# Kernel optimization log

Measured on AMD Instinct MI355X. Metric: run time of the kernel, lower is better.

Reference implementation:

```python
import jax, jax.numpy as jnp
import numpy as np

HIDDEN = 4096
N_HEADS = 32
N_KV_HEADS = 2
HEAD_DIM = 128          # hidden // n_heads
ROT_DIM = HEAD_DIM // 2  # partial rotary (ChatGLM style)
ROPE_THETA = 10000.0
Q_SIZE = N_HEADS * HEAD_DIM
KV_SIZE = N_KV_HEADS * HEAD_DIM
SCALE = HEAD_DIM ** -0.5
T = 2048


def setup_inputs() -> dict:
    key = jax.random.key(0)
    k1, k2, k3, k4 = jax.random.split(key, 4)
    hidden_states = jax.random.normal(k1, (T, HIDDEN), dtype=jnp.float32)
    positions = jnp.arange(T, dtype=jnp.int64) if jax.config.jax_enable_x64 else jnp.arange(T, dtype=jnp.int32)
    w_qkv = jax.random.normal(k2, (Q_SIZE + 2 * KV_SIZE, HIDDEN), dtype=jnp.float32) * 0.02
    b_qkv = jax.random.normal(k3, (Q_SIZE + 2 * KV_SIZE,), dtype=jnp.float32) * 0.02
    w_dense = jax.random.normal(k4, (HIDDEN, Q_SIZE), dtype=jnp.float32) * 0.02
    return {"hidden_states": hidden_states, "positions": positions,
            "w_qkv": w_qkv, "b_qkv": b_qkv, "w_dense": w_dense}


def _apply_rope(x, positions):
    # x: [T, H, HEAD_DIM]; interleaved (is_neox_style=False) partial rotary on first ROT_DIM dims
    half = ROT_DIM // 2
    inv_freq = 1.0 / (ROPE_THETA ** (jnp.arange(0, half, dtype=jnp.float32) * 2.0 / ROT_DIM))
    freqs = positions.astype(jnp.float32)[:, None] * inv_freq[None, :]   # [T, half]
    cos = jnp.cos(freqs)[:, None, :]  # [T, 1, half]
    sin = jnp.sin(freqs)[:, None, :]
    x_rot = x[..., :ROT_DIM]
    x_pass = x[..., ROT_DIM:]
    x1 = x_rot[..., 0::2]
    x2 = x_rot[..., 1::2]
    o1 = x1 * cos - x2 * sin
    o2 = x2 * cos + x1 * sin
    rot = jnp.stack([o1, o2], axis=-1).reshape(x_rot.shape)  # re-interleave
    return jnp.concatenate([rot, x_pass], axis=-1)


def reference(hidden_states, positions, w_qkv, b_qkv, w_dense):
    # QKV projection (bias from add_qkv_bias=True)
    qkv = hidden_states @ w_qkv.T + b_qkv                     # [T, 4608]
    q = qkv[:, :Q_SIZE].reshape(T, N_HEADS, HEAD_DIM)
    k = qkv[:, Q_SIZE:Q_SIZE + KV_SIZE].reshape(T, N_KV_HEADS, HEAD_DIM)
    v = qkv[:, Q_SIZE + KV_SIZE:].reshape(T, N_KV_HEADS, HEAD_DIM)

    q = _apply_rope(q, positions)
    k = _apply_rope(k, positions)

    # GQA: expand 2 kv heads -> 32 q heads (each kv head serves 16 q heads)
    rep = N_HEADS // N_KV_HEADS
    k = jnp.repeat(k, rep, axis=1)                            # [T, 32, 128]
    v = jnp.repeat(v, rep, axis=1)

    # Causal scaled dot-product attention
    scores = jnp.einsum('thd,shd->hts', q, k) * SCALE         # [H, T, T]
    causal = positions[:, None] >= positions[None, :]          # [T, T]
    scores = jnp.where(causal[None, :, :], scores, jnp.finfo(scores.dtype).min)
    probs = jax.nn.softmax(scores, axis=-1)
    attn = jnp.einsum('hts,shd->thd', probs, v).reshape(T, Q_SIZE)

    # Output projection (no bias: add_bias_linear=False)
    return attn @ w_dense.T
```

## Files before the change

kernel.cpp:

```cpp
#include <hip/hip_runtime.h>
#include <cstdint>
#include <math.h>

typedef __bf16 bf16;
typedef __bf16 bf16x8 __attribute__((ext_vector_type(8)));
typedef __bf16 bf16x4 __attribute__((ext_vector_type(4)));
typedef float f32x4 __attribute__((ext_vector_type(4)));

#define T_SEQ 2048
#define HID   4096
#define NQH   32
#define NKVH  2
#define HD    128
#define NQKV  4608
#define ATT_SCALE 0.08838834764831845f

#define VMCNT(n) asm volatile("s_waitcnt vmcnt(" #n ")" ::: "memory")

__device__ __forceinline__ void load_lds16(const void* g, void* l) {
    auto gp = (const __attribute__((address_space(1))) unsigned int*)(uintptr_t)g;
    auto lp = (__attribute__((address_space(3))) unsigned int*)(unsigned int)(uintptr_t)l;
    __builtin_amdgcn_global_load_lds(gp, lp, 16, 0, 0);
}

__device__ __forceinline__ f32x4 mfma16(bf16x8 a, bf16x8 b, f32x4 c) {
    return __builtin_amdgcn_mfma_f32_16x16x32_bf16(a, b, c, 0, 0, 0);
}

__device__ __forceinline__ bf16x8 cvt8(const float* s) {
    float4 a = *(const float4*)(s);
    float4 b = *(const float4*)(s + 4);
    bf16x8 o;
    o[0] = (bf16)a.x; o[1] = (bf16)a.y; o[2] = (bf16)a.z; o[3] = (bf16)a.w;
    o[4] = (bf16)b.x; o[5] = (bf16)b.y; o[6] = (bf16)b.z; o[7] = (bf16)b.w;
    return o;
}

__global__ void cvt2_kernel(const float* __restrict__ s0, bf16* __restrict__ d0, long n0,
                            const float* __restrict__ s1, bf16* __restrict__ d1, long n1) {
    const long nv = (n0 + n1) >> 3;
    for (long v = (long)blockIdx.x * 256 + threadIdx.x; v < nv; v += (long)gridDim.x * 256) {
        long i = v << 3;
        if (i < n0) *(bf16x8*)(d0 + i) = cvt8(s0 + i);
        else        *(bf16x8*)(d1 + (i - n0)) = cvt8(s1 + (i - n0));
    }
}

__global__ void cvt_f32_bf16_kernel(const float* __restrict__ x, bf16* __restrict__ y) {
    size_t i = ((size_t)blockIdx.x * 256 + threadIdx.x) * 8;
    *(bf16x8*)(y + i) = cvt8(x + i);
}

template <int OUT_BF16, int HAS_BIAS>
__global__ __launch_bounds__(256) void gemm_bt(const bf16* __restrict__ A,
                                               const bf16* __restrict__ B,
                                               const float* __restrict__ bias,
                                               void* __restrict__ Cout,
                                               int M, int N, int K) {
    __shared__ __align__(16) char sA[2][16384];
    __shared__ __align__(16) char sB[2][16384];
    const int tid = threadIdx.x;
    const int wid = tid >> 6, l = tid & 63, l4 = l >> 4, l16 = l & 15;
    const int wm = wid >> 1, wn = wid & 1;
    const int bm = blockIdx.x * 128, bn = blockIdx.y * 128;

    f32x4 acc[4][4] = {};

    auto stage = [&](int buf, int k0) {
#pragma unroll
        for (int c4 = 0; c4 < 4; ++c4) {
            int ch = c4 * 256 + tid;
            int row = ch >> 3, cch = ch & 7;
            int scc = cch ^ (row & 7);
            load_lds16(A + (size_t)(bm + row) * K + k0 + scc * 8,
                       sA[buf] + c4 * 4096 + wid * 1024);
        }
#pragma unroll
        for (int c4 = 0; c4 < 4; ++c4) {
            int ch = c4 * 256 + tid;
            int row = ch >> 3, cch = ch & 7;
            int scc = cch ^ (row & 7);
            load_lds16(B + (size_t)(bn + row) * K + k0 + scc * 8,
                       sB[buf] + c4 * 4096 + wid * 1024);
        }
    };

    stage(0, 0);
    const int NT = K >> 6;
    int cur = 0;
    for (int t = 0; t < NT; ++t) {
        __builtin_amdgcn_s_barrier();
        __builtin_amdgcn_sched_barrier(0);
        if (t + 1 < NT) {
            stage(cur ^ 1, (t + 1) * 64);
            VMCNT(8);
        } else {
            VMCNT(0);
        }
        __builtin_amdgcn_s_barrier();
        __builtin_amdgcn_sched_barrier(0);

        const char* pA = sA[cur];
        const char* pB = sB[cur];
#pragma unroll
        for (int ks = 0; ks < 2; ++ks) {
            bf16x8 af[4], bfr[4];
#pragma unroll
            for (int mi = 0; mi < 4; ++mi) {
                int row = wm * 64 + mi * 16 + l16;
                af[mi] = *(const bf16x8*)(pA + row * 128 + ((ks * 64 + l4 * 16) ^ ((row & 7) << 4)));
            }
#pragma unroll
            for (int ni = 0; ni < 4; ++ni) {
                int row = wn * 64 + ni * 16 + l16;
                bfr[ni] = *(const bf16x8*)(pB + row * 128 + ((ks * 64 + l4 * 16) ^ ((row & 7) << 4)));
            }
#pragma unroll
            for (int mi = 0; mi < 4; ++mi)
#pragma unroll
                for (int ni = 0; ni < 4; ++ni)
                    acc[mi][ni] = mfma16(af[mi], bfr[ni], acc[mi][ni]);
        }
        cur ^= 1;
    }

#pragma unroll
    for (int mi = 0; mi < 4; ++mi)
#pragma unroll
        for (int ni = 0; ni < 4; ++ni) {
            const int col = bn + wn * 64 + ni * 16 + l16;
            float bv = HAS_BIAS ? bias[col] : 0.0f;
#pragma unroll
            for (int r = 0; r < 4; ++r) {
                const int row = bm + wm * 64 + mi * 16 + l4 * 4 + r;
                float val = acc[mi][ni][r] + bv;
                if (OUT_BF16)
                    ((bf16*)Cout)[(size_t)row * N + col] = (bf16)val;
                else
                    ((float*)Cout)[(size_t)row * N + col] = val;
            }
        }
}

__global__ void rope_qk_kernel(const bf16* __restrict__ qkv,
                               bf16* __restrict__ qheads, bf16* __restrict__ kheads) {
    const int t = blockIdx.x;
    const int g = blockIdx.y;
    const int sub = threadIdx.x >> 6;
    const int l = threadIdx.x & 63;
    const bf16* src;
    bf16* dst;
    if (g < 8) {
        int hh = g * 4 + sub;
        src = qkv + (size_t)t * NQKV + hh * HD;
        dst = qheads + ((size_t)hh * T_SEQ + t) * HD;
    } else {
        if (sub >= 2) return;
        src = qkv + (size_t)t * NQKV + HID + sub * HD;
        dst = kheads + ((size_t)sub * T_SEQ + t) * HD;
    }
    if (l < 32) {
        const int i = l;
        float x1 = (float)src[2 * i], x2 = (float)src[2 * i + 1];
        float fr = (float)t * exp2f((float)i * (-13.287712379549449f / 32.0f));
        float sn = sinf(fr), cs = cosf(fr);
        dst[2 * i] = (bf16)(x1 * cs - x2 * sn);
        dst[2 * i + 1] = (bf16)(x2 * cs + x1 * sn);
    } else {
        const int j = l - 32;
        dst[64 + 2 * j] = src[64 + 2 * j];
        dst[64 + 2 * j + 1] = src[64 + 2 * j + 1];
    }
}

__global__ void v_trans_kernel(const bf16* __restrict__ qkv, bf16* __restrict__ vt) {
    const int t0 = blockIdx.x * 64;
    const int kvh = blockIdx.y;
    const int tid = threadIdx.x;
#pragma unroll
    for (int it = 0; it < 4; ++it) {
        int ch = it * 256 + tid;
        int d = ch >> 3, tc = ch & 7;
        int t = t0 + tc * 8;
        const bf16* src = qkv + (size_t)t * NQKV + 4352 + kvh * HD + d;
        bf16x8 v;
#pragma unroll
        for (int i = 0; i < 8; ++i) v[i] = src[(size_t)i * NQKV];
        *(bf16x8*)(vt + ((size_t)kvh * HD + d) * T_SEQ + t) = v;
    }
}

__global__ __launch_bounds__(256, 1) void attn_fwd_kernel(const bf16* __restrict__ qh,
                                                          const bf16* __restrict__ kh,
                                                          const bf16* __restrict__ vt,
                                                          bf16* __restrict__ attnb) {
    __shared__ __align__(16) char sK[2][16384];
    __shared__ __align__(16) char sV[16384];
    __shared__ __align__(16) char sP[4][4096];
    const int tid = threadIdx.x;
    const int wid = tid >> 6, l = tid & 63, l4 = l >> 4, l16 = l & 15;
    const int b = blockIdx.x;
    const int qb = 15 - (b >> 5);
    const int h = b & 31, kvh = h >> 4;
    const int qbase = qb * 128 + wid * 32;

    auto stageK = [&](int buf, int kt) {
#pragma unroll
        for (int c4 = 0; c4 < 4; ++c4) {
            int ch = c4 * 256 + tid;
            int row = ch >> 4, cc = ch & 15;
            load_lds16(kh + ((size_t)kvh * T_SEQ + kt * 64 + row) * HD + (cc ^ (row & 7)) * 8,
                       sK[buf] + c4 * 4096 + wid * 1024);
        }
    };
    auto stageV = [&](int kt) {
#pragma unroll
        for (int c4 = 0; c4 < 4; ++c4) {
            int ch = c4 * 256 + tid;
            int row = ch >> 3, cc = ch & 7;
            load_lds16(vt + ((size_t)kvh * HD + row) * T_SEQ + kt * 64 + (cc ^ (row & 7)) * 8,
                       sV + c4 * 4096 + wid * 1024);
        }
    };

    bf16x8 qf[2][4];
#pragma unroll
    for (int rg = 0; rg < 2; ++rg) {
        const bf16* qp = qh + ((size_t)h * T_SEQ + qbase + rg * 16 + l16) * HD + l4 * 8;
#pragma unroll
        for (int f = 0; f < 4; ++f) qf[rg][f] = *(const bf16x8*)(qp + f * 32);
    }
    VMCNT(0);
    stageK(0, 0);

    f32x4 o[2][8] = {};
    float mr[2][4], lr[2][4];
#pragma unroll
    for (int rg = 0; rg < 2; ++rg)
#pragma unroll
        for (int r = 0; r < 4; ++r) { mr[rg][r] = -INFINITY; lr[rg][r] = 0.f; }

    const int nt = 2 * qb + 2;
    int cur = 0;
    for (int kt = 0; kt < nt; ++kt) {
        const bool havenext = (kt + 1 < nt);
        __builtin_amdgcn_s_barrier();
        __builtin_amdgcn_sched_barrier(0);
        stageV(kt);
        if (havenext) stageK(cur ^ 1, kt + 1);
        if (havenext) { VMCNT(16); } else { VMCNT(8); }
        __builtin_amdgcn_s_barrier();
        __builtin_amdgcn_sched_barrier(0);

        const bool active = (kt * 64) <= (qbase + 31);
        if (active) {
            f32x4 s[2][4] = {};
            __builtin_amdgcn_s_setprio(1);
#pragma unroll
            for (int ct = 0; ct < 4; ++ct)
#pragma unroll
                for (int ks = 0; ks < 4; ++ks) {
                    int row = ct * 16 + l16;
                    bf16x8 kf = *(const bf16x8*)(sK[cur] + row * 256 + ((ks * 64 + l4 * 16) ^ ((row & 7) << 4)));
                    s[0][ct] = mfma16(qf[0][ks], kf, s[0][ct]);
                    s[1][ct] = mfma16(qf[1][ks], kf, s[1][ct]);
                }
            __builtin_amdgcn_s_setprio(0);

            const bool diag = (kt * 64 + 63 > qbase);
            float sv[2][4][4];
#pragma unroll
            for (int rg = 0; rg < 2; ++rg)
#pragma unroll
                for (int ct = 0; ct < 4; ++ct)
#pragma unroll
                    for (int r = 0; r < 4; ++r) {
                        float x = s[rg][ct][r] * ATT_SCALE;
                        if (diag && (kt * 64 + ct * 16 + l16) > (qbase + rg * 16 + l4 * 4 + r)) x = -INFINITY;
                        sv[rg][ct][r] = x;
                    }

            float pmx[2][4];
            bool ok = true;
#pragma unroll
            for (int rg = 0; rg < 2; ++rg)
#pragma unroll
                for (int r = 0; r < 4; ++r) {
                    pmx[rg][r] = fmaxf(fmaxf(sv[rg][0][r], sv[rg][1][r]), fmaxf(sv[rg][2][r], sv[rg][3][r]));
                    ok = ok && (pmx[rg][r] <= mr[rg][r] + 8.0f);
                }
            if (!__all(ok)) {
#pragma unroll
                for (int rg = 0; rg < 2; ++rg)
#pragma unroll
                    for (int r = 0; r < 4; ++r) {
                        float mx = pmx[rg][r];
                        mx = fmaxf(mx, __shfl_xor(mx, 1));
                        mx = fmaxf(mx, __shfl_xor(mx, 2));
                        mx = fmaxf(mx, __shfl_xor(mx, 4));
                        mx = fmaxf(mx, __shfl_xor(mx, 8));
                        if (mx > mr[rg][r]) {
                            float al = __expf(mr[rg][r] - mx);
                            mr[rg][r] = mx;
                            lr[rg][r] *= al;
#pragma unroll
                            for (int n2 = 0; n2 < 8; ++n2) o[rg][n2][r] *= al;
                        }
                    }
            }
#pragma unroll
            for (int rg = 0; rg < 2; ++rg)
#pragma unroll
                for (int r = 0; r < 4; ++r) {
                    float ps = 0.f;
                    const int prow = rg * 16 + l4 * 4 + r;
#pragma unroll
                    for (int ct = 0; ct < 4; ++ct) {
                        float p = __expf(sv[rg][ct][r] - mr[rg][r]);
                        ps += p;
                        *(bf16*)(sP[wid] + prow * 128 + (((ct * 16 + l16) * 2) ^ ((prow & 7) << 4))) = (bf16)p;
                    }
                    lr[rg][r] += ps;
                }
        }

        if (havenext) { VMCNT(8); } else { VMCNT(0); }
        __builtin_amdgcn_s_barrier();
        __builtin_amdgcn_sched_barrier(0);

        if (active) {
#pragma unroll
            for (int ks = 0; ks < 2; ++ks) {
                bf16x8 pa0 = *(const bf16x8*)(sP[wid] + l16 * 128 + ((ks * 64 + l4 * 16) ^ ((l16 & 7) << 4)));
                bf16x8 pa1 = *(const bf16x8*)(sP[wid] + (16 + l16) * 128 + ((ks * 64 + l4 * 16) ^ ((l16 & 7) << 4)));
                __builtin_amdgcn_s_setprio(1);
#pragma unroll
                for (int n2 = 0; n2 < 8; ++n2) {
                    int vrow = n2 * 16 + l16;
                    bf16x8 vf = *(const bf16x8*)(sV + vrow * 128 + ((ks * 64 + l4 * 16) ^ ((vrow & 7) << 4)));
                    o[0][n2] = mfma16(pa0, vf, o[0][n2]);
                    o[1][n2] = mfma16(pa1, vf, o[1][n2]);
                }
                __builtin_amdgcn_s_setprio(0);
            }
        }
        cur ^= 1;
    }

    float inv[2][4];
#pragma unroll
    for (int rg = 0; rg < 2; ++rg)
#pragma unroll
        for (int r = 0; r < 4; ++r) {
            float s2 = lr[rg][r];
            s2 += __shfl_xor(s2, 1);
            s2 += __shfl_xor(s2, 2);
            s2 += __shfl_xor(s2, 4);
            s2 += __shfl_xor(s2, 8);
            inv[rg][r] = 1.0f / s2;
        }
#pragma unroll
    for (int rg = 0; rg < 2; ++rg)
#pragma unroll
        for (int n2 = 0; n2 < 8; ++n2)
#pragma unroll
            for (int r = 0; r < 4; ++r) {
                int row = qb * 128 + wid * 32 + rg * 16 + l4 * 4 + r;
                int col = h * HD + n2 * 16 + l16;
                attnb[(size_t)row * HID + col] = (bf16)(o[rg][n2][r] * inv[rg][r]);
            }
}

extern "C" void kernel_launch(void* const* d_in, const int* in_sizes, int n_in,
                              void* d_out, int out_size, void* d_ws, size_t ws_size,
                              hipStream_t stream) {
    const float* hs = (const float*)d_in[0];
    const float* wqkv = (const float*)d_in[2];
    const float* bqkv = (const float*)d_in[3];
    const float* wdense = (const float*)d_in[4];
    float* out = (float*)d_out;

    char* ws = (char*)d_ws;
    bf16* wqkvb   = (bf16*)(ws + 0);
    bf16* hb      = (bf16*)(ws + 37748736);
    bf16* qkvb    = (bf16*)(ws + 54525952);
    bf16* qhp     = (bf16*)(ws + 0);
    bf16* khp     = (bf16*)(ws + 16777216);
    bf16* vtp     = (bf16*)(ws + 17825792);
    bf16* wdenseb = (bf16*)(ws + 18874368);
    bf16* attnb   = (bf16*)(ws + 54525952);
    (void)in_sizes; (void)n_in; (void)out_size; (void)ws_size;

    cvt2_kernel<<<2048, 256, 0, stream>>>(hs, hb, (long)T_SEQ * HID,
                                          wqkv, wqkvb, (long)NQKV * HID);

    dim3 g1(T_SEQ / 128, NQKV / 128);
    gemm_bt<1, 1><<<g1, 256, 0, stream>>>(hb, wqkvb, bqkv, (void*)qkvb, T_SEQ, NQKV, HID);

    cvt_f32_bf16_kernel<<<(HID * HID) / 2048, 256, 0, stream>>>(wdense, wdenseb);

    rope_qk_kernel<<<dim3(T_SEQ, 9), 256, 0, stream>>>(qkvb, qhp, khp);
    v_trans_kernel<<<dim3(T_SEQ / 64, NKVH), 256, 0, stream>>>(qkvb, vtp);

    attn_fwd_kernel<<<512, 256, 0, stream>>>(qhp, khp, vtp, attnb);

    dim3 g2(T_SEQ / 128, HID / 128);
    gemm_bt<0, 0><<<g2, 256, 0, stream>>>(attnb, wdenseb, nullptr, (void*)out, T_SEQ, HID, HID);
}
```

Before: 326.4 us.

## Drop LDS staging in attention, load K/V directly, fuse w_dense conversion

The attention kernel stops staging K and V through double-buffered LDS with barriers. Each wave now loads its K and V fragments straight from global memory into registers and computes a per-wave trip count, so no block-level synchronisation is needed. The separate w_dense f32-to-bf16 conversion kernel is folded into the tail of the attention kernel, saving one launch, and the occupancy hint of one block per CU is dropped. In exchange, K/V tiles that four waves could share are fetched redundantly from global or L2 memory, with no async prefetch to hide the load latency.

```diff
diff --git a/kernel.cpp b/kernel.cpp
--- a/kernel.cpp
+++ b/kernel.cpp
@@ -44,11 +44,6 @@
         if (i < n0) *(bf16x8*)(d0 + i) = cvt8(s0 + i);
         else        *(bf16x8*)(d1 + (i - n0)) = cvt8(s1 + (i - n0));
     }
-}
-
-__global__ void cvt_f32_bf16_kernel(const float* __restrict__ x, bf16* __restrict__ y) {
-    size_t i = ((size_t)blockIdx.x * 256 + threadIdx.x) * 8;
-    *(bf16x8*)(y + i) = cvt8(x + i);
 }
 
 template <int OUT_BF16, int HAS_BIAS>
@@ -190,12 +185,12 @@
     }
 }
 
-__global__ __launch_bounds__(256, 1) void attn_fwd_kernel(const bf16* __restrict__ qh,
-                                                          const bf16* __restrict__ kh,
-                                                          const bf16* __restrict__ vt,
-                                                          bf16* __restrict__ attnb) {
-    __shared__ __align__(16) char sK[2][16384];
-    __shared__ __align__(16) char sV[16384];
+__global__ __launch_bounds__(256) void attn_fwd_kernel(const bf16* __restrict__ qh,
+                                                       const bf16* __restrict__ kh,
+                                                       const bf16* __restrict__ vt,
+                                                       bf16* __restrict__ attnb,
+                                                       const float* __restrict__ wdense,
+                                                       bf16* __restrict__ wdenseb) {
     __shared__ __align__(16) char sP[4][4096];
     const int tid = threadIdx.x;
     const int wid = tid >> 6, l = tid & 63, l4 = l >> 4, l16 = l & 15;
@@ -204,25 +199,6 @@
     const int h = b & 31, kvh = h >> 4;
     const int qbase = qb * 128 + wid * 32;
 
-    auto stageK = [&](int buf, int kt) {
-#pragma unroll
-        for (int c4 = 0; c4 < 4; ++c4) {
-            int ch = c4 * 256 + tid;
-            int row = ch >> 4, cc = ch & 15;
-            load_lds16(kh + ((size_t)kvh * T_SEQ + kt * 64 + row) * HD + (cc ^ (row & 7)) * 8,
-                       sK[buf] + c4 * 4096 + wid * 1024);
-        }
-    };
-    auto stageV = [&](int kt) {
-#pragma unroll
-        for (int c4 = 0; c4 < 4; ++c4) {
-            int ch = c4 * 256 + tid;
-            int row = ch >> 3, cc = ch & 7;
-            load_lds16(vt + ((size_t)kvh * HD + row) * T_SEQ + kt * 64 + (cc ^ (row & 7)) * 8,
-                       sV + c4 * 4096 + wid * 1024);
-        }
-    };
-
     bf16x8 qf[2][4];
 #pragma unroll
     for (int rg = 0; rg < 2; ++rg) {
@@ -230,8 +206,6 @@
 #pragma unroll
         for (int f = 0; f < 4; ++f) qf[rg][f] = *(const bf16x8*)(qp + f * 32);
     }
-    VMCNT(0);
-    stageK(0, 0);
 
     f32x4 o[2][8] = {};
     float mr[2][4], lr[2][4];
@@ -240,111 +214,101 @@
 #pragma unroll
         for (int r = 0; r < 4; ++r) { mr[rg][r] = -INFINITY; lr[rg][r] = 0.f; }
 
-    const int nt = 2 * qb + 2;
-    int cur = 0;
+    const int nt = (qbase + 31) / 64 + 1;
+    const bf16* kbase = kh + (size_t)kvh * T_SEQ * HD;
+    const bf16* vbase = vt + (size_t)kvh * HD * T_SEQ;
+
     for (int kt = 0; kt < nt; ++kt) {
-        const bool havenext = (kt + 1 < nt);
-        __builtin_amdgcn_s_barrier();
-        __builtin_amdgcn_sched_barrier(0);
-        stageV(kt);
-        if (havenext) stageK(cur ^ 1, kt + 1);
-        if (havenext) { VMCNT(16); } else { VMCNT(8); }
-        __builtin_amdgcn_s_barrier();
-        __builtin_amdgcn_sched_barrier(0);
-
-        const bool active = (kt * 64) <= (qbase + 31);
-        if (active) {
-            f32x4 s[2][4] = {};
+        bf16x8 kf[4][4];
+#pragma unroll
+        for (int ct = 0; ct < 4; ++ct)
+#pragma unroll
+            for (int ks = 0; ks < 4; ++ks)
+                kf[ct][ks] = *(const bf16x8*)(kbase + (size_t)(kt * 64 + ct * 16 + l16) * HD + ks * 32 + l4 * 8);
+
+        f32x4 s[2][4] = {};
+        __builtin_amdgcn_s_setprio(1);
+#pragma unroll
+        for (int ct = 0; ct < 4; ++ct)
+#pragma unroll
+            for (int ks = 0; ks < 4; ++ks) {
+                s[0][ct] = mfma16(qf[0][ks], kf[ct][ks], s[0][ct]);
+                s[1][ct] = mfma16(qf[1][ks], kf[ct][ks], s[1][ct]);
+            }
+        __builtin_amdgcn_s_setprio(0);
+
+        const bool diag = (kt * 64 + 63 > qbase);
+        float sv[2][4][4];
+#pragma unroll
+        for (int rg = 0; rg < 2; ++rg)
+#pragma unroll
+            for (int ct = 0; ct < 4; ++ct)
+#pragma unroll
+                for (int r = 0; r < 4; ++r) {
+                    float x = s[rg][ct][r] * ATT_SCALE;
+                    if (diag && (kt * 64 + ct * 16 + l16) > (qbase + rg * 16 + l4 * 4 + r)) x = -INFINITY;
+                    sv[rg][ct][r] = x;
+                }
+
+        float pmx[2][4];
+        bool ok = true;
+#pragma unroll
+        for (int rg = 0; rg < 2; ++rg)
+#pragma unroll
+            for (int r = 0; r < 4; ++r) {
+                pmx[rg][r] = fmaxf(fmaxf(sv[rg][0][r], sv[rg][1][r]), fmaxf(sv[rg][2][r], sv[rg][3][r]));
+                ok = ok && (pmx[rg][r] <= mr[rg][r] + 8.0f);
+            }
+        if (!__all(ok)) {
+#pragma unroll
+            for (int rg = 0; rg < 2; ++rg)
+#pragma unroll
+                for (int r = 0; r < 4; ++r) {
+                    float mx = pmx[rg][r];
+                    mx = fmaxf(mx, __shfl_xor(mx, 1));
+                    mx = fmaxf(mx, __shfl_xor(mx, 2));
+                    mx = fmaxf(mx, __shfl_xor(mx, 4));
+                    mx = fmaxf(mx, __shfl_xor(mx, 8));
+                    if (mx > mr[rg][r]) {
+                        float al = __expf(mr[rg][r] - mx);
+                        mr[rg][r] = mx;
+                        lr[rg][r] *= al;
+#pragma unroll
+                        for (int n2 = 0; n2 < 8; ++n2) o[rg][n2][r] *= al;
+                    }
+                }
+        }
+#pragma unroll
+        for (int rg = 0; rg < 2; ++rg)
+#pragma unroll
+            for (int r = 0; r < 4; ++r) {
+                float ps = 0.f;
+                const int prow = rg * 16 + l4 * 4 + r;
+#pragma unroll
+                for (int ct = 0; ct < 4; ++ct) {
+                    float p = __expf(sv[rg][ct][r] - mr[rg][r]);
+                    ps += p;
+                    *(bf16*)(sP[wid] + prow * 128 + (((ct * 16 + l16) * 2) ^ ((prow & 7) << 4))) = (bf16)p;
+                }
+                lr[rg][r] += ps;
+            }
+
+#pragma unroll
+        for (int ks = 0; ks < 2; ++ks) {
+            bf16x8 pa0 = *(const bf16x8*)(sP[wid] + l16 * 128 + ((ks * 64 + l4 * 16) ^ ((l16 & 7) << 4)));
+            bf16x8 pa1 = *(const bf16x8*)(sP[wid] + (16 + l16) * 128 + ((ks * 64 + l4 * 16) ^ ((l16 & 7) << 4)));
+            bf16x8 vf[8];
+#pragma unroll
+            for (int n2 = 0; n2 < 8; ++n2)
+                vf[n2] = *(const bf16x8*)(vbase + (size_t)(n2 * 16 + l16) * T_SEQ + kt * 64 + ks * 32 + l4 * 8);
             __builtin_amdgcn_s_setprio(1);
 #pragma unroll
-            for (int ct = 0; ct < 4; ++ct)
-#pragma unroll
-                for (int ks = 0; ks < 4; ++ks) {
-                    int row = ct * 16 + l16;
-                    bf16x8 kf = *(const bf16x8*)(sK[cur] + row * 256 + ((ks * 64 + l4 * 16) ^ ((row & 7) << 4)));
-                    s[0][ct] = mfma16(qf[0][ks], kf, s[0][ct]);
-                    s[1][ct] = mfma16(qf[1][ks], kf, s[1][ct]);
-                }
+            for (int n2 = 0; n2 < 8; ++n2) {
+                o[0][n2] = mfma16(pa0, vf[n2], o[0][n2]);
+                o[1][n2] = mfma16(pa1, vf[n2], o[1][n2]);
+            }
             __builtin_amdgcn_s_setprio(0);
-
-            const bool diag = (kt * 64 + 63 > qbase);
-            float sv[2][4][4];
-#pragma unroll
-            for (int rg = 0; rg < 2; ++rg)
-#pragma unroll
-                for (int ct = 0; ct < 4; ++ct)
-#pragma unroll
-                    for (int r = 0; r < 4; ++r) {
-                        float x = s[rg][ct][r] * ATT_SCALE;
-                        if (diag && (kt * 64 + ct * 16 + l16) > (qbase + rg * 16 + l4 * 4 + r)) x = -INFINITY;
-                        sv[rg][ct][r] = x;
-                    }
-
-            float pmx[2][4];
-            bool ok = true;
-#pragma unroll
-            for (int rg = 0; rg < 2; ++rg)
-#pragma unroll
-                for (int r = 0; r < 4; ++r) {
-                    pmx[rg][r] = fmaxf(fmaxf(sv[rg][0][r], sv[rg][1][r]), fmaxf(sv[rg][2][r], sv[rg][3][r]));
-                    ok = ok && (pmx[rg][r] <= mr[rg][r] + 8.0f);
-                }
-            if (!__all(ok)) {
-#pragma unroll
-                for (int rg = 0; rg < 2; ++rg)
-#pragma unroll
-                    for (int r = 0; r < 4; ++r) {
-                        float mx = pmx[rg][r];
-                        mx = fmaxf(mx, __shfl_xor(mx, 1));
-                        mx = fmaxf(mx, __shfl_xor(mx, 2));
-                        mx = fmaxf(mx, __shfl_xor(mx, 4));
-                        mx = fmaxf(mx, __shfl_xor(mx, 8));
-                        if (mx > mr[rg][r]) {
-                            float al = __expf(mr[rg][r] - mx);
-                            mr[rg][r] = mx;
-                            lr[rg][r] *= al;
-#pragma unroll
-                            for (int n2 = 0; n2 < 8; ++n2) o[rg][n2][r] *= al;
-                        }
-                    }
-            }
-#pragma unroll
-            for (int rg = 0; rg < 2; ++rg)
-#pragma unroll
-                for (int r = 0; r < 4; ++r) {
-                    float ps = 0.f;
-                    const int prow = rg * 16 + l4 * 4 + r;
-#pragma unroll
-                    for (int ct = 0; ct < 4; ++ct) {
-                        float p = __expf(sv[rg][ct][r] - mr[rg][r]);
-                        ps += p;
-                        *(bf16*)(sP[wid] + prow * 128 + (((ct * 16 + l16) * 2) ^ ((prow & 7) << 4))) = (bf16)p;
-                    }
-                    lr[rg][r] += ps;
-                }
-        }
-
-        if (havenext) { VMCNT(8); } else { VMCNT(0); }
-        __builtin_amdgcn_s_barrier();
-        __builtin_amdgcn_sched_barrier(0);
-
-        if (active) {
-#pragma unroll
-            for (int ks = 0; ks < 2; ++ks) {
-                bf16x8 pa0 = *(const bf16x8*)(sP[wid] + l16 * 128 + ((ks * 64 + l4 * 16) ^ ((l16 & 7) << 4)));
-                bf16x8 pa1 = *(const bf16x8*)(sP[wid] + (16 + l16) * 128 + ((ks * 64 + l4 * 16) ^ ((l16 & 7) << 4)));
-                __builtin_amdgcn_s_setprio(1);
-#pragma unroll
-                for (int n2 = 0; n2 < 8; ++n2) {
-                    int vrow = n2 * 16 + l16;
-                    bf16x8 vf = *(const bf16x8*)(sV + vrow * 128 + ((ks * 64 + l4 * 16) ^ ((vrow & 7) << 4)));
-                    o[0][n2] = mfma16(pa0, vf, o[0][n2]);
-                    o[1][n2] = mfma16(pa1, vf, o[1][n2]);
-                }
-                __builtin_amdgcn_s_setprio(0);
-            }
-        }
-        cur ^= 1;
+        }
     }
 
     float inv[2][4];
@@ -369,6 +333,12 @@
                 int col = h * HD + n2 * 16 + l16;
                 attnb[(size_t)row * HID + col] = (bf16)(o[rg][n2][r] * inv[rg][r]);
             }
+
+#pragma unroll 1
+    for (int it = 0; it < 16; ++it) {
+        long v = ((long)it * 512 + b) * 256 + tid;
+        *(bf16x8*)(wdenseb + v * 8) = cvt8(wdense + v * 8);
+    }
 }
 
 extern "C" void kernel_launch(void* const* d_in, const int* in_sizes, int n_in,
@@ -397,12 +367,10 @@
     dim3 g1(T_SEQ / 128, NQKV / 128);
     gemm_bt<1, 1><<<g1, 256, 0, stream>>>(hb, wqkvb, bqkv, (void*)qkvb, T_SEQ, NQKV, HID);
 
-    cvt_f32_bf16_kernel<<<(HID * HID) / 2048, 256, 0, stream>>>(wdense, wdenseb);
-
     rope_qk_kernel<<<dim3(T_SEQ, 9), 256, 0, stream>>>(qkvb, qhp, khp);
     v_trans_kernel<<<dim3(T_SEQ / 64, NKVH), 256, 0, stream>>>(qkvb, vtp);
 
-    attn_fwd_kernel<<<512, 256, 0, stream>>>(qhp, khp, vtp, attnb);
+    attn_fwd_kernel<<<512, 256, 0, stream>>>(qhp, khp, vtp, attnb, wdense, wdenseb);
 
     dim3 g2(T_SEQ / 128, HID / 128);
     gemm_bt<0, 0><<<g2, 256, 0, stream>>>(attnb, wdenseb, nullptr, (void*)out, T_SEQ, HID, HID);
```

After: 369.2 us. +13.1%, slower.

## Fuse RoPE and V transpose into QKV GEMM epilogue

Applied to the files above, without the earlier changes.

The QKV GEMM epilogue now writes bias-added results straight into head-major Q/K buffers, applying interleaved RoPE to the first 64 dims via lane shuffles, and writes V directly transposed. This removes the separate rope and v-transpose kernels and the round trip through an intermediate qkv buffer. The cost is sin/cos evaluation and scattered 2-byte stores in the epilogue, plus a rearranged workspace layout.

```diff
diff --git a/kernel.cpp b/kernel.cpp
--- a/kernel.cpp
+++ b/kernel.cpp
@@ -51,11 +51,14 @@
     *(bf16x8*)(y + i) = cvt8(x + i);
 }
 
-template <int OUT_BF16, int HAS_BIAS>
+template <int MODE, int HAS_BIAS>
 __global__ __launch_bounds__(256) void gemm_bt(const bf16* __restrict__ A,
                                                const bf16* __restrict__ B,
                                                const float* __restrict__ bias,
                                                void* __restrict__ Cout,
+                                               bf16* __restrict__ qh,
+                                               bf16* __restrict__ kh,
+                                               bf16* __restrict__ vtr,
                                                int M, int N, int K) {
     __shared__ __align__(16) char sA[2][16384];
     __shared__ __align__(16) char sB[2][16384];
@@ -124,69 +127,74 @@
         cur ^= 1;
     }
 
-#pragma unroll
-    for (int mi = 0; mi < 4; ++mi)
-#pragma unroll
-        for (int ni = 0; ni < 4; ++ni) {
-            const int col = bn + wn * 64 + ni * 16 + l16;
-            float bv = HAS_BIAS ? bias[col] : 0.0f;
-#pragma unroll
-            for (int r = 0; r < 4; ++r) {
-                const int row = bm + wm * 64 + mi * 16 + l4 * 4 + r;
-                float val = acc[mi][ni][r] + bv;
-                if (OUT_BF16)
-                    ((bf16*)Cout)[(size_t)row * N + col] = (bf16)val;
-                else
-                    ((float*)Cout)[(size_t)row * N + col] = val;
-            }
-        }
-}
-
-__global__ void rope_qk_kernel(const bf16* __restrict__ qkv,
-                               bf16* __restrict__ qheads, bf16* __restrict__ kheads) {
-    const int t = blockIdx.x;
-    const int g = blockIdx.y;
-    const int sub = threadIdx.x >> 6;
-    const int l = threadIdx.x & 63;
-    const bf16* src;
-    bf16* dst;
-    if (g < 8) {
-        int hh = g * 4 + sub;
-        src = qkv + (size_t)t * NQKV + hh * HD;
-        dst = qheads + ((size_t)hh * T_SEQ + t) * HD;
+    if (MODE == 0) {
+#pragma unroll
+        for (int mi = 0; mi < 4; ++mi)
+#pragma unroll
+            for (int ni = 0; ni < 4; ++ni) {
+                const int col = bn + wn * 64 + ni * 16 + l16;
+                float bv = HAS_BIAS ? bias[col] : 0.0f;
+#pragma unroll
+                for (int r = 0; r < 4; ++r) {
+                    const int row = bm + wm * 64 + mi * 16 + l4 * 4 + r;
+                    ((float*)Cout)[(size_t)row * N + col] = acc[mi][ni][r] + bv;
+                }
+            }
     } else {
-        if (sub >= 2) return;
-        src = qkv + (size_t)t * NQKV + HID + sub * HD;
-        dst = kheads + ((size_t)sub * T_SEQ + t) * HD;
-    }
-    if (l < 32) {
-        const int i = l;
-        float x1 = (float)src[2 * i], x2 = (float)src[2 * i + 1];
-        float fr = (float)t * exp2f((float)i * (-13.287712379549449f / 32.0f));
-        float sn = sinf(fr), cs = cosf(fr);
-        dst[2 * i] = (bf16)(x1 * cs - x2 * sn);
-        dst[2 * i + 1] = (bf16)(x2 * cs + x1 * sn);
-    } else {
-        const int j = l - 32;
-        dst[64 + 2 * j] = src[64 + 2 * j];
-        dst[64 + 2 * j + 1] = src[64 + 2 * j + 1];
-    }
-}
-
-__global__ void v_trans_kernel(const bf16* __restrict__ qkv, bf16* __restrict__ vt) {
-    const int t0 = blockIdx.x * 64;
-    const int kvh = blockIdx.y;
-    const int tid = threadIdx.x;
-#pragma unroll
-    for (int it = 0; it < 4; ++it) {
-        int ch = it * 256 + tid;
-        int d = ch >> 3, tc = ch & 7;
-        int t = t0 + tc * 8;
-        const bf16* src = qkv + (size_t)t * NQKV + 4352 + kvh * HD + d;
-        bf16x8 v;
-#pragma unroll
-        for (int i = 0; i < 8; ++i) v[i] = src[(size_t)i * NQKV];
-        *(bf16x8*)(vt + ((size_t)kvh * HD + d) * T_SEQ + t) = v;
+        const int by = blockIdx.y;
+        if (by >= 34) {
+            bf16* dst = vtr + (size_t)(by - 34) * HD * T_SEQ;
+#pragma unroll
+            for (int mi = 0; mi < 4; ++mi)
+#pragma unroll
+                for (int ni = 0; ni < 4; ++ni) {
+                    const int cl = wn * 64 + ni * 16 + l16;
+                    const float bv = bias[bn + cl];
+                    bf16x4 pk;
+#pragma unroll
+                    for (int r = 0; r < 4; ++r) pk[r] = (bf16)(acc[mi][ni][r] + bv);
+                    const int t0 = bm + wm * 64 + mi * 16 + l4 * 4;
+                    *(bf16x4*)(dst + (size_t)cl * T_SEQ + t0) = pk;
+                }
+        } else {
+            bf16* dst = (by < 32) ? qh + (size_t)by * T_SEQ * HD
+                                  : kh + (size_t)(by - 32) * T_SEQ * HD;
+            if (wn == 0) {
+#pragma unroll
+                for (int ni = 0; ni < 4; ++ni) {
+                    const int cl = ni * 16 + l16;
+                    const float bv = bias[bn + cl];
+                    const int i = cl >> 1;
+                    const float invf = exp2f((float)i * (-13.287712379549449f / 32.0f));
+                    const bool even = (l16 & 1) == 0;
+#pragma unroll
+                    for (int mi = 0; mi < 4; ++mi)
+#pragma unroll
+                        for (int r = 0; r < 4; ++r) {
+                            const int t = bm + wm * 64 + mi * 16 + l4 * 4 + r;
+                            float v = acc[mi][ni][r] + bv;
+                            float p = __shfl_xor(v, 1);
+                            float fr = (float)t * invf;
+                            float sn = sinf(fr), cs = cosf(fr);
+                            float ov = even ? (v * cs - p * sn) : (v * cs + p * sn);
+                            dst[(size_t)t * HD + cl] = (bf16)ov;
+                        }
+                }
+            } else {
+#pragma unroll
+                for (int mi = 0; mi < 4; ++mi)
+#pragma unroll
+                    for (int ni = 0; ni < 4; ++ni) {
+                        const int cl = 64 + ni * 16 + l16;
+                        const float bv = bias[bn + cl];
+#pragma unroll
+                        for (int r = 0; r < 4; ++r) {
+                            const int t = bm + wm * 64 + mi * 16 + l4 * 4 + r;
+                            dst[(size_t)t * HD + cl] = (bf16)(acc[mi][ni][r] + bv);
+                        }
+                    }
+            }
+        }
     }
 }
 
@@ -383,27 +391,25 @@
     char* ws = (char*)d_ws;
     bf16* wqkvb   = (bf16*)(ws + 0);
     bf16* hb      = (bf16*)(ws + 37748736);
-    bf16* qkvb    = (bf16*)(ws + 54525952);
-    bf16* qhp     = (bf16*)(ws + 0);
-    bf16* khp     = (bf16*)(ws + 16777216);
-    bf16* vtp     = (bf16*)(ws + 17825792);
-    bf16* wdenseb = (bf16*)(ws + 18874368);
-    bf16* attnb   = (bf16*)(ws + 54525952);
+    bf16* qhp     = (bf16*)(ws + 54525952);
+    bf16* khp     = (bf16*)(ws + 71303168);
+    bf16* vtp     = (bf16*)(ws + 72351744);
+    bf16* wdenseb = (bf16*)(ws + 0);
+    bf16* attnb   = (bf16*)(ws + 37748736);
     (void)in_sizes; (void)n_in; (void)out_size; (void)ws_size;
 
     cvt2_kernel<<<2048, 256, 0, stream>>>(hs, hb, (long)T_SEQ * HID,
                                           wqkv, wqkvb, (long)NQKV * HID);
 
     dim3 g1(T_SEQ / 128, NQKV / 128);
-    gemm_bt<1, 1><<<g1, 256, 0, stream>>>(hb, wqkvb, bqkv, (void*)qkvb, T_SEQ, NQKV, HID);
+    gemm_bt<2, 1><<<g1, 256, 0, stream>>>(hb, wqkvb, bqkv, nullptr,
+                                          qhp, khp, vtp, T_SEQ, NQKV, HID);
 
     cvt_f32_bf16_kernel<<<(HID * HID) / 2048, 256, 0, stream>>>(wdense, wdenseb);
 
-    rope_qk_kernel<<<dim3(T_SEQ, 9), 256, 0, stream>>>(qkvb, qhp, khp);
-    v_trans_kernel<<<dim3(T_SEQ / 64, NKVH), 256, 0, stream>>>(qkvb, vtp);
-
     attn_fwd_kernel<<<512, 256, 0, stream>>>(qhp, khp, vtp, attnb);
 
     dim3 g2(T_SEQ / 128, HID / 128);
-    gemm_bt<0, 0><<<g2, 256, 0, stream>>>(attnb, wdenseb, nullptr, (void*)out, T_SEQ, HID, HID);
-}
+    gemm_bt<0, 0><<<g2, 256, 0, stream>>>(attnb, wdenseb, nullptr, (void*)out,
+                                          nullptr, nullptr, nullptr, T_SEQ, HID, HID);
+}
```

Result: slower. 347.1 us (+6.3%).
